# Kernel optimization log

Hardware: AMD Instinct MI355X
Metric: run time of the kernel (lower is better)

Reference implementation:

```python
import jax, jax.numpy as jnp
import numpy as np

B, S, E = 4, 2048, 1024

def setup_inputs() -> dict:
    key = jax.random.key(0)
    ks = jax.random.split(key, 4)
    scale = 1.0 / np.sqrt(E)
    x = jax.random.normal(ks[0], (B, S, E), dtype=jnp.float32)
    Wq = jax.random.normal(ks[1], (E, E), dtype=jnp.float32) * scale
    Wk = jax.random.normal(ks[2], (E, E), dtype=jnp.float32) * scale
    Wv = jax.random.normal(ks[3], (E, E), dtype=jnp.float32) * scale
    bq = jnp.zeros((E,), dtype=jnp.float32)
    bk = jnp.zeros((E,), dtype=jnp.float32)
    bv = jnp.zeros((E,), dtype=jnp.float32)
    # causal mask: 1 where attention allowed, 0 where blocked (masked_fill(mask==0, -inf))
    mask = jnp.tril(jnp.ones((S, S), dtype=jnp.int32))
    return {"x": x, "mask": mask, "Wq": Wq, "bq": bq, "Wk": Wk, "bk": bk, "Wv": Wv, "bv": bv}

def reference(x, mask, Wq, bq, Wk, bk, Wv, bv):
    # x: (B, S, E); mask: (S, S) int, 0 -> -inf. Matches torch nn.Linear: x @ W.T + b
    Q = jnp.einsum('bse,fe->bsf', x, Wq) + bq
    K = jnp.einsum('bse,fe->bsf', x, Wk) + bk
    V = jnp.einsum('bse,fe->bsf', x, Wv) + bv
    inv_sqrt_e = 1.0 / jnp.sqrt(jnp.asarray(x.shape[-1], dtype=x.dtype))
    scores = jnp.einsum('bqe,bke->bqk', Q, K) * inv_sqrt_e  # (B, S, S)
    scores = jnp.where(mask[None, :, :] == 0, jnp.asarray(-jnp.inf, scores.dtype), scores)
    attn = jax.nn.softmax(scores, axis=-1)
    out = jnp.einsum('bqk,bke->bqe', attn, V)  # (B, S, E)
    return out
```

## Files before the change

### kernel.cpp

```cpp
#include <hip/hip_runtime.h>

#define B_ 4
#define S_ 2048
#define E_ 1024

typedef __attribute__((ext_vector_type(8))) short short8;
typedef __attribute__((ext_vector_type(4))) float f32x4;

__device__ __forceinline__ unsigned short f2bu(float f) {
  unsigned u = __builtin_bit_cast(unsigned, f);
  u = (u + 0x7FFFu + ((u >> 16) & 1u)) >> 16;
  return (unsigned short)u;
}

__device__ __forceinline__ void gload_lds16(const void* g, void* l) {
  __builtin_amdgcn_global_load_lds(
      (const __attribute__((address_space(1))) void*)g,
      (__attribute__((address_space(3))) void*)l, 16, 0, 0);
}

__global__ __launch_bounds__(256) void cvt_w3(
    const float* __restrict__ w0, const float* __restrict__ w1,
    const float* __restrict__ w2, unsigned short* __restrict__ out, int n) {
  int z = blockIdx.z;
  const float* in = (z == 0) ? w0 : (z == 1) ? w1 : w2;
  int i = blockIdx.x * 256 + threadIdx.x;
  if (i * 4 >= n) return;
  float4 v = ((const float4*)in)[i];
  ushort4 o;
  o.x = f2bu(v.x); o.y = f2bu(v.y); o.z = f2bu(v.z); o.w = f2bu(v.w);
  ((ushort4*)(out + (long)z * n))[i] = o;
}

__global__ __launch_bounds__(256) void zden(float* __restrict__ d) {
  ((float4*)d)[blockIdx.x * 256 + threadIdx.x] = float4{0.f, 0.f, 0.f, 0.f};
}

__global__ __launch_bounds__(256, 3) void k_qkv(
    const float* __restrict__ X, const unsigned short* __restrict__ W,
    const float* __restrict__ bq, const float* __restrict__ bk,
    const float* __restrict__ bv,
    unsigned short* __restrict__ Qo, unsigned short* __restrict__ Ko,
    unsigned short* __restrict__ Vt) {
  __shared__ unsigned short lA[128 * 64];
  __shared__ unsigned short lB[128 * 64];
  int bid = blockIdx.y * 24 + blockIdx.x;
  int nb = (bid & 7) * 192 + (bid >> 3);
  int bm = nb / 24, bn = nb % 24;

  int tid = threadIdx.x;
  int l = tid & 63, w = tid >> 6;
  int wm = w >> 1, wn = w & 1;

  const unsigned short* Bb = W + (long)bn * 128 * E_;
  int srow = l >> 3, schunk = (l & 7) * 8;
  const unsigned short* gb[4];
  unsigned short* lbd[4];
#pragma unroll
  for (int i = 0; i < 4; i++) {
    int seg = i * 4 + w;
    gb[i] = Bb + (long)(seg * 8 + srow) * E_ + schunk;
    lbd[i] = &lB[seg * 512];
  }

  const float* Xb = X + (long)bm * 128 * E_ + (l & 7) * 8;
  int arw = w * 8 + (l >> 3);
  int awoff = w * 512 + l * 8;
  float4 st[4][2];

  int aoff[4], boff[4];
#pragma unroll
  for (int i = 0; i < 4; i++) {
    aoff[i] = (wm * 64 + i * 16 + (l & 15)) * 64 + (l >> 4) * 8;
    boff[i] = (wn * 64 + i * 16 + (l & 15)) * 64 + (l >> 4) * 8;
  }

#pragma unroll
  for (int j = 0; j < 4; j++) {
    const float* p = Xb + (long)(j * 32 + arw) * E_;
    st[j][0] = *(const float4*)p;
    st[j][1] = *(const float4*)(p + 4);
  }

  f32x4 acc[4][4] = {};

  for (int k0 = 0; k0 < E_; k0 += 64) {
    __syncthreads();
#pragma unroll
    for (int j = 0; j < 4; j++) {
      short8 pk;
      pk[0] = (short)f2bu(st[j][0].x); pk[1] = (short)f2bu(st[j][0].y);
      pk[2] = (short)f2bu(st[j][0].z); pk[3] = (short)f2bu(st[j][0].w);
      pk[4] = (short)f2bu(st[j][1].x); pk[5] = (short)f2bu(st[j][1].y);
      pk[6] = (short)f2bu(st[j][1].z); pk[7] = (short)f2bu(st[j][1].w);
      *(short8*)&lA[j * 2048 + awoff] = pk;
    }
#pragma unroll
    for (int i = 0; i < 4; i++) { gload_lds16(gb[i], lbd[i]); gb[i] += 64; }
    __syncthreads();

    if (k0 + 64 < E_) {
#pragma unroll
      for (int j = 0; j < 4; j++) {
        const float* p = Xb + (long)(j * 32 + arw) * E_ + (k0 + 64);
        st[j][0] = *(const float4*)p;
        st[j][1] = *(const float4*)(p + 4);
      }
    }

#pragma unroll
    for (int kk = 0; kk < 2; kk++) {
      short8 af[4], bf[4];
#pragma unroll
      for (int i = 0; i < 4; i++) af[i] = *(const short8*)&lA[aoff[i] + kk * 32];
#pragma unroll
      for (int j = 0; j < 4; j++) bf[j] = *(const short8*)&lB[boff[j] + kk * 32];
#pragma unroll
      for (int i = 0; i < 4; i++)
#pragma unroll
        for (int j = 0; j < 4; j++)
          acc[i][j] = __builtin_amdgcn_mfma_f32_16x16x32_bf16(af[i], bf[j], acc[i][j], 0, 0, 0);
    }
  }

  int rh = l >> 4, cl = l & 15;
  long rowbase = (long)bm * 128 + wm * 64 + rh * 4;
  int colbase = bn * 128 + wn * 64 + cl;
  int seg = bn >> 3;
  const float* bias = (seg == 0) ? bq : (seg == 1) ? bk : bv;
#pragma unroll
  for (int j = 0; j < 4; j++) {
    int c = colbase + j * 16;
    int cl_ = c & 1023;
    float bv_ = bias[cl_];
#pragma unroll
    for (int i = 0; i < 4; i++) {
      long r0 = rowbase + i * 16;
      f32x4 v = acc[i][j];
      if (seg < 2) {
        unsigned short* Ch = (seg == 0) ? Qo : Ko;
#pragma unroll
        for (int t = 0; t < 4; t++)
          Ch[(r0 + t) * (long)E_ + cl_] = f2bu(v[t] + bv_);
      } else {
        ushort4 pk;
        pk.x = f2bu(v[0] + bv_);
        pk.y = f2bu(v[1] + bv_);
        pk.z = f2bu(v[2] + bv_);
        pk.w = f2bu(v[3] + bv_);
        *(ushort4*)(Vt + (long)cl_ * (B_ * S_) + r0) = pk;
      }
    }
  }
}

template<int MODE>
__device__ __forceinline__ void gemm_body(
    const unsigned short* __restrict__ A, long sAz, int lda,
    const unsigned short* __restrict__ B, long sBz, int ldb,
    void* __restrict__ C0, long sCz, int ldc, int K, float scale,
    float* __restrict__ denom,
    unsigned short* lA, unsigned short* lB, int bm, int bn, int bz) {
  constexpr int BK = 64;
  const unsigned short* Ab = A + (long)bz * sAz + (long)bm * 128 * lda;
  const unsigned short* Bb = B + (long)bz * sBz + (long)bn * 128 * ldb;
  int Keff = (MODE == 2) ? min(K, (bm + 1) * 128) : K;

  int tid = threadIdx.x;
  int l = tid & 63, w = tid >> 6;
  int wm = w >> 1, wn = w & 1;

  int srow = l >> 3;
  int schunk = (l & 7) * 8;
  const unsigned short* ga[4];
  const unsigned short* gb[4];
  unsigned short* lad[4];
  unsigned short* lbd[4];
#pragma unroll
  for (int i = 0; i < 4; i++) {
    int seg = i * 4 + w;
    int row = seg * 8 + srow;
    ga[i] = Ab + (long)row * lda + schunk;
    gb[i] = Bb + (long)row * ldb + schunk;
    lad[i] = &lA[seg * 512];
    lbd[i] = &lB[seg * 512];
  }
  int aoff[4], boff[4];
#pragma unroll
  for (int i = 0; i < 4; i++) {
    aoff[i] = (wm * 64 + i * 16 + (l & 15)) * BK + (l >> 4) * 8;
    boff[i] = (wn * 64 + i * 16 + (l & 15)) * BK + (l >> 4) * 8;
  }

  f32x4 acc[4][4] = {};

  for (int k0 = 0; k0 < Keff; k0 += BK) {
    __syncthreads();
#pragma unroll
    for (int i = 0; i < 4; i++) {
      gload_lds16(ga[i], lad[i]);
      gload_lds16(gb[i], lbd[i]);
    }
#pragma unroll
    for (int i = 0; i < 4; i++) { ga[i] += BK; gb[i] += BK; }
    __syncthreads();
#pragma unroll
    for (int kk = 0; kk < 2; kk++) {
      short8 af[4], bf[4];
#pragma unroll
      for (int i = 0; i < 4; i++) af[i] = *(const short8*)&lA[aoff[i] + kk * 32];
#pragma unroll
      for (int j = 0; j < 4; j++) bf[j] = *(const short8*)&lB[boff[j] + kk * 32];
#pragma unroll
      for (int i = 0; i < 4; i++)
#pragma unroll
        for (int j = 0; j < 4; j++)
          acc[i][j] = __builtin_amdgcn_mfma_f32_16x16x32_bf16(af[i], bf[j], acc[i][j], 0, 0, 0);
    }
  }

  int rh = l >> 4, cl = l & 15;
  long rowbase = (long)bm * 128 + wm * 64 + rh * 4;
  int colbase = bn * 128 + wn * 64 + cl;

  if constexpr (MODE == 1) {
    unsigned short* Ph = (unsigned short*)C0 + (long)bz * sCz;
    float rs[4][4] = {};
#pragma unroll
    for (int i = 0; i < 4; i++) {
      int r0 = (int)rowbase + i * 16;
#pragma unroll
      for (int t = 0; t < 4; t++) {
        int r = r0 + t;
#pragma unroll
        for (int j = 0; j < 4; j++) {
          int c = colbase + j * 16;
          float p = (c <= r) ? __expf(acc[i][j][t] * scale) : 0.f;
          Ph[(long)r * ldc + c] = f2bu(p);
          rs[i][t] += p;
        }
      }
    }
#pragma unroll
    for (int i = 0; i < 4; i++)
#pragma unroll
      for (int t = 0; t < 4; t++) {
        float s = rs[i][t];
        s += __shfl_xor(s, 1);
        s += __shfl_xor(s, 2);
        s += __shfl_xor(s, 4);
        s += __shfl_xor(s, 8);
        rs[i][t] = s;
      }
    if ((l & 15) == 0) {
      float* dz = denom + (long)bz * S_;
#pragma unroll
      for (int i = 0; i < 4; i++)
#pragma unroll
        for (int t = 0; t < 4; t++)
          atomicAdd(&dz[(int)rowbase + i * 16 + t], rs[i][t]);
    }
  } else {
    float* Cf = (float*)C0 + (long)bz * sCz;
    const float* dz = denom + (long)bz * S_;
    float rdn[4][4];
#pragma unroll
    for (int i = 0; i < 4; i++)
#pragma unroll
      for (int t = 0; t < 4; t++)
        rdn[i][t] = 1.0f / dz[(int)rowbase + i * 16 + t];
#pragma unroll
    for (int j = 0; j < 4; j++) {
      int c = colbase + j * 16;
#pragma unroll
      for (int i = 0; i < 4; i++) {
        long r0 = rowbase + i * 16;
        f32x4 v = acc[i][j];
#pragma unroll
        for (int t = 0; t < 4; t++)
          Cf[(r0 + t) * (long)ldc + c] = v[t] * rdn[i][t];
      }
    }
  }
}

__global__ __launch_bounds__(256, 3) void k_scores(
    const unsigned short* __restrict__ Q, const unsigned short* __restrict__ K,
    unsigned short* __restrict__ P, float* __restrict__ denom) {
  __shared__ unsigned short lA[128 * 64];
  __shared__ unsigned short lB[128 * 64];
  int t0 = blockIdx.x;
  int t = (t0 & 7) * 17 + (t0 >> 3);
  int bm = (int)((sqrtf(8.f * t + 1.f) - 1.f) * 0.5f);
  while ((bm + 1) * (bm + 2) / 2 <= t) bm++;
  while (bm * (bm + 1) / 2 > t) bm--;
  int bn = t - bm * (bm + 1) / 2;
  gemm_body<1>(Q, (long)S_ * E_, E_, K, (long)S_ * E_, E_,
               P, (long)S_ * S_, S_, E_, 0.03125f, denom,
               lA, lB, bm, bn, blockIdx.z);
}

__global__ __launch_bounds__(256, 3) void k_pv(
    const unsigned short* __restrict__ P, const unsigned short* __restrict__ Vt,
    float* __restrict__ out, const float* __restrict__ denom) {
  __shared__ unsigned short lA[128 * 64];
  __shared__ unsigned short lB[128 * 64];
  int bm = 15 - blockIdx.y;
  gemm_body<2>(P, (long)S_ * S_, S_, Vt, (long)S_, B_ * S_,
               out, (long)S_ * E_, E_, S_, 1.f, (float*)denom,
               lA, lB, bm, blockIdx.x, blockIdx.z);
}

extern "C" void kernel_launch(void* const* d_in, const int* in_sizes, int n_in,
                              void* d_out, int out_size, void* d_ws, size_t ws_size,
                              hipStream_t stream) {
  const float* x  = (const float*)d_in[0];
  const float* Wq = (const float*)d_in[2];
  const float* bq = (const float*)d_in[3];
  const float* Wk = (const float*)d_in[4];
  const float* bk = (const float*)d_in[5];
  const float* Wv = (const float*)d_in[6];
  const float* bv = (const float*)d_in[7];
  float* out = (float*)d_out;

  const long NX = (long)B_ * S_ * E_;
  const long NW = (long)E_ * E_;
  unsigned short* wqb = (unsigned short*)d_ws;
  unsigned short* Qb  = wqb + 3 * NW;
  unsigned short* Kb  = Qb + NX;
  unsigned short* Vtb = Kb + NX;
  unsigned short* Pb  = Vtb + NX;
  float* denom = (float*)(Pb + (long)B_ * S_ * S_);

  cvt_w3<<<dim3(1024, 1, 3), 256, 0, stream>>>(Wq, Wk, Wv, wqb, (int)NW);
  zden<<<8, 256, 0, stream>>>(denom);

  k_qkv<<<dim3(24, 64), 256, 0, stream>>>(x, wqb, bq, bk, bv, Qb, Kb, Vtb);

  k_scores<<<dim3(136, 1, 4), 256, 0, stream>>>(Qb, Kb, Pb, denom);

  k_pv<<<dim3(8, 16, 4), 256, 0, stream>>>(Pb, Vtb, out, denom);
}
```

Before: 170.6 us.

## Pre-convert X to bf16 and load both GEMM operands directly into LDS

Adds a separate kernel that converts the fp32 input X to bf16 in workspace. The QKV projection then streams both A and B tiles with global_load_lds instead of loading fp32 X into registers and converting inside the GEMM loop. The block tile grows to 256x128 with 512 threads (8 waves) and the grid is halved. In exchange there is an extra full pass over X plus a bf16 copy in workspace, and the launch bounds (512, 6) ask for an occupancy that could force register pressure or spills.

```diff
diff --git a/kernel.cpp b/kernel.cpp
--- a/kernel.cpp
+++ b/kernel.cpp
@@ -17,6 +17,16 @@
   __builtin_amdgcn_global_load_lds(
       (const __attribute__((address_space(1))) void*)g,
       (__attribute__((address_space(3))) void*)l, 16, 0, 0);
+}
+
+__global__ __launch_bounds__(256) void cvt_f32_bf16(
+    const float* __restrict__ in, unsigned short* __restrict__ out, int n) {
+  int i = blockIdx.x * 256 + threadIdx.x;
+  if (i * 4 >= n) return;
+  float4 v = ((const float4*)in)[i];
+  ushort4 o;
+  o.x = f2bu(v.x); o.y = f2bu(v.y); o.z = f2bu(v.z); o.w = f2bu(v.w);
+  ((ushort4*)out)[i] = o;
 }
 
 __global__ __launch_bounds__(256) void cvt_w3(
@@ -36,37 +46,42 @@
   ((float4*)d)[blockIdx.x * 256 + threadIdx.x] = float4{0.f, 0.f, 0.f, 0.f};
 }
 
-__global__ __launch_bounds__(256, 3) void k_qkv(
-    const float* __restrict__ X, const unsigned short* __restrict__ W,
+__global__ __launch_bounds__(512, 6) void k_qkv(
+    const unsigned short* __restrict__ A, const unsigned short* __restrict__ W,
     const float* __restrict__ bq, const float* __restrict__ bk,
     const float* __restrict__ bv,
     unsigned short* __restrict__ Qo, unsigned short* __restrict__ Ko,
     unsigned short* __restrict__ Vt) {
-  __shared__ unsigned short lA[128 * 64];
+  __shared__ unsigned short lA[256 * 64];
   __shared__ unsigned short lB[128 * 64];
   int bid = blockIdx.y * 24 + blockIdx.x;
-  int nb = (bid & 7) * 192 + (bid >> 3);
+  int nb = (bid & 7) * 96 + (bid >> 3);
   int bm = nb / 24, bn = nb % 24;
 
   int tid = threadIdx.x;
   int l = tid & 63, w = tid >> 6;
   int wm = w >> 1, wn = w & 1;
 
+  const unsigned short* Ab = A + (long)bm * 256 * E_;
   const unsigned short* Bb = W + (long)bn * 128 * E_;
+
   int srow = l >> 3, schunk = (l & 7) * 8;
-  const unsigned short* gb[4];
-  unsigned short* lbd[4];
+  const unsigned short* ga[4];
+  unsigned short* lad[4];
 #pragma unroll
   for (int i = 0; i < 4; i++) {
-    int seg = i * 4 + w;
+    int seg = i * 8 + w;
+    ga[i] = Ab + (long)(seg * 8 + srow) * E_ + schunk;
+    lad[i] = &lA[seg * 512];
+  }
+  const unsigned short* gb[2];
+  unsigned short* lbd[2];
+#pragma unroll
+  for (int i = 0; i < 2; i++) {
+    int seg = i * 8 + w;
     gb[i] = Bb + (long)(seg * 8 + srow) * E_ + schunk;
     lbd[i] = &lB[seg * 512];
   }
-
-  const float* Xb = X + (long)bm * 128 * E_ + (l & 7) * 8;
-  int arw = w * 8 + (l >> 3);
-  int awoff = w * 512 + l * 8;
-  float4 st[4][2];
 
   int aoff[4], boff[4];
 #pragma unroll
@@ -75,39 +90,15 @@
     boff[i] = (wn * 64 + i * 16 + (l & 15)) * 64 + (l >> 4) * 8;
   }
 
-#pragma unroll
-  for (int j = 0; j < 4; j++) {
-    const float* p = Xb + (long)(j * 32 + arw) * E_;
-    st[j][0] = *(const float4*)p;
-    st[j][1] = *(const float4*)(p + 4);
-  }
-
   f32x4 acc[4][4] = {};
 
   for (int k0 = 0; k0 < E_; k0 += 64) {
     __syncthreads();
 #pragma unroll
-    for (int j = 0; j < 4; j++) {
-      short8 pk;
-      pk[0] = (short)f2bu(st[j][0].x); pk[1] = (short)f2bu(st[j][0].y);
-      pk[2] = (short)f2bu(st[j][0].z); pk[3] = (short)f2bu(st[j][0].w);
-      pk[4] = (short)f2bu(st[j][1].x); pk[5] = (short)f2bu(st[j][1].y);
-      pk[6] = (short)f2bu(st[j][1].z); pk[7] = (short)f2bu(st[j][1].w);
-      *(short8*)&lA[j * 2048 + awoff] = pk;
-    }
-#pragma unroll
-    for (int i = 0; i < 4; i++) { gload_lds16(gb[i], lbd[i]); gb[i] += 64; }
+    for (int i = 0; i < 4; i++) { gload_lds16(ga[i], lad[i]); ga[i] += 64; }
+#pragma unroll
+    for (int i = 0; i < 2; i++) { gload_lds16(gb[i], lbd[i]); gb[i] += 64; }
     __syncthreads();
-
-    if (k0 + 64 < E_) {
-#pragma unroll
-      for (int j = 0; j < 4; j++) {
-        const float* p = Xb + (long)(j * 32 + arw) * E_ + (k0 + 64);
-        st[j][0] = *(const float4*)p;
-        st[j][1] = *(const float4*)(p + 4);
-      }
-    }
-
 #pragma unroll
     for (int kk = 0; kk < 2; kk++) {
       short8 af[4], bf[4];
@@ -124,7 +115,7 @@
   }
 
   int rh = l >> 4, cl = l & 15;
-  long rowbase = (long)bm * 128 + wm * 64 + rh * 4;
+  long rowbase = (long)bm * 256 + wm * 64 + rh * 4;
   int colbase = bn * 128 + wn * 64 + cl;
   int seg = bn >> 3;
   const float* bias = (seg == 0) ? bq : (seg == 1) ? bk : bv;
@@ -325,17 +316,19 @@
 
   const long NX = (long)B_ * S_ * E_;
   const long NW = (long)E_ * E_;
-  unsigned short* wqb = (unsigned short*)d_ws;
+  unsigned short* xb  = (unsigned short*)d_ws;
+  unsigned short* wqb = xb + NX;
   unsigned short* Qb  = wqb + 3 * NW;
   unsigned short* Kb  = Qb + NX;
   unsigned short* Vtb = Kb + NX;
   unsigned short* Pb  = Vtb + NX;
   float* denom = (float*)(Pb + (long)B_ * S_ * S_);
 
+  cvt_f32_bf16<<<8192, 256, 0, stream>>>(x, xb, (int)NX);
   cvt_w3<<<dim3(1024, 1, 3), 256, 0, stream>>>(Wq, Wk, Wv, wqb, (int)NW);
   zden<<<8, 256, 0, stream>>>(denom);
 
-  k_qkv<<<dim3(24, 64), 256, 0, stream>>>(x, wqb, bq, bk, bv, Qb, Kb, Vtb);
+  k_qkv<<<dim3(24, 32), 512, 0, stream>>>(xb, wqb, bq, bk, bv, Qb, Kb, Vtb);
 
   k_scores<<<dim3(136, 1, 4), 256, 0, stream>>>(Qb, Kb, Pb, denom);
 
```

New measurement: 573.6 us. 3.36x slower.
